# Kernel optimization log

Hardware: AMD Instinct MI355X
Metric: run time of the kernel (lower is better)

The kernel has to match this reference:

```python
import jax, jax.numpy as jnp
import numpy as np

DIM_IN = 1024
DIM_OUT = 1024
BATCH = 4
SEQ = 2048


def setup_inputs() -> dict:
    key = jax.random.key(0)
    kx, kq, kk, kv = jax.random.split(key, 4)
    scale = 1.0 / np.sqrt(DIM_IN)
    x = jax.random.normal(kx, (BATCH, SEQ, DIM_IN), dtype=jnp.float32)
    # Weights stored as [dim_in, dim_out] (transpose of torch Linear's [out, in]);
    # y = x @ W is equivalent math to torch's x @ W_t.T
    Wq = jax.random.normal(kq, (DIM_IN, DIM_OUT), dtype=jnp.float32) * scale
    Wk = jax.random.normal(kk, (DIM_IN, DIM_OUT), dtype=jnp.float32) * scale
    Wv = jax.random.normal(kv, (DIM_IN, DIM_OUT), dtype=jnp.float32) * scale
    return {"x": x, "Wq": Wq, "Wk": Wk, "Wv": Wv}


def reference(x, Wq, Wk, Wv):
    # x: [b, s, d_in]; single-head causal self-attention (dropout=0 -> identity)
    q = jnp.einsum("bsd,de->bse", x, Wq)
    k = jnp.einsum("bsd,de->bse", x, Wk)
    v = jnp.einsum("bsd,de->bse", x, Wv)
    dim_k = k.shape[-1]
    scores = jnp.einsum("bqe,bke->bqk", q, k) / jnp.sqrt(jnp.float32(dim_k))
    s = x.shape[1]
    causal = jnp.tril(jnp.ones((s, s), dtype=bool))  # True = keep
    scores = jnp.where(causal[None, :, :], scores, -jnp.inf)
    weights = jax.nn.softmax(scores, axis=-1)
    context = jnp.einsum("bqk,bke->bqe", weights, v)
    return context
```

## Files before the change

kernel.cpp:

```cpp
#include <hip/hip_runtime.h>
#include <cstdint>
#include <cstddef>
#include <type_traits>

typedef unsigned short u16;
typedef __bf16 bf16x8 __attribute__((ext_vector_type(8)));
typedef float f32x4 __attribute__((ext_vector_type(4)));

__device__ inline u16 f2b(float f) {
    uint32_t u = __builtin_bit_cast(uint32_t, f);
    u += 0x7FFFu + ((u >> 16) & 1u);
    return (u16)(u >> 16);
}

__device__ inline void gl2lds16(const u16* g, u16* l) {
    __builtin_amdgcn_global_load_lds(
        (const __attribute__((address_space(1))) void*)g,
        (__attribute__((address_space(3))) void*)l, 16, 0, 0);
}

template<int N> __device__ __forceinline__ void waitvm() {
    asm volatile("s_waitcnt vmcnt(%0)" :: "n"(N) : "memory");
}
__device__ __forceinline__ void bar() {
    asm volatile("" ::: "memory");
    __builtin_amdgcn_s_barrier();
    asm volatile("" ::: "memory");
}

__global__ void convert_x_kernel(const float* __restrict__ x, u16* __restrict__ xb) {
    size_t i = ((size_t)blockIdx.x * 256 + threadIdx.x) * 4;
    float4 v = *(const float4*)(x + i);
    uint2 pack;
    pack.x = (uint32_t)f2b(v.x) | ((uint32_t)f2b(v.y) << 16);
    pack.y = (uint32_t)f2b(v.z) | ((uint32_t)f2b(v.w) << 16);
    *(uint2*)(xb + i) = pack;
}

__global__ void transpose_w_kernel(const float* __restrict__ Wq,
                                   const float* __restrict__ Wk,
                                   const float* __restrict__ Wv,
                                   u16* __restrict__ QKWT, u16* __restrict__ WvT) {
    __shared__ u16 t[32][33];
    const int z = blockIdx.z;
    const float* W = (z == 0) ? Wq : ((z == 1) ? Wk : Wv);
    u16* dst = (z == 0) ? QKWT : ((z == 1) ? QKWT + 1024 * 1024 : WvT);
    const float scale = (z == 0) ? 0.03125f : 1.0f;
    const int bx = blockIdx.x * 32;
    const int by = blockIdx.y * 32;
    const int tx = threadIdx.x, ty = threadIdx.y;
    #pragma unroll
    for (int r = 0; r < 32; r += 8)
        t[ty + r][tx] = f2b(W[(size_t)(by + ty + r) * 1024 + bx + tx] * scale);
    __syncthreads();
    #pragma unroll
    for (int r = 0; r < 32; r += 8)
        dst[(size_t)(bx + ty + r) * 1024 + (by + tx)] = t[tx][ty + r];
}

template<int NB, int EPI>
__device__ __forceinline__ void gemm8p(
    char* __restrict__ sm,
    const u16* __restrict__ A, int lda,
    const u16* __restrict__ B, int ldb,
    char* __restrict__ Cb, int ldc,
    int m0, int n0, int Kloc, float* __restrict__ lrow)
{
    constexpr int BREG  = NB / 2;
    constexpr int BUFSZ = (2 + BREG) * 16384;
    constexpr int BOFF  = 2 * 16384;
    constexpr int WVM   = NB;

    const int tid  = threadIdx.x;
    const int lane = tid & 63, wave = tid >> 6;
    const int wm = wave >> 2, wn = wave & 3;
    const int fl = lane & 15, fh = lane >> 4;

    const int sx = ((fl & 4) << 3) ^ ((fl & 1) << 6);

    const int rr0 = tid >> 3;
    const int kc  = ((tid & 7) * 8) ^ ((rr0 & 4) << 2) ^ ((rr0 & 1) << 5);
    const u16* sA0a = A + (size_t)(m0 + rr0) * lda + kc;
    const u16* sA0b = A + (size_t)(m0 + rr0 + 64) * lda + kc;
    const u16* sA1a = sA0a + (size_t)128 * lda;
    const u16* sA1b = sA0b + (size_t)128 * lda;
    const u16* sB0a = B + (size_t)(n0 + rr0) * ldb + kc;
    const u16* sB0b = B + (size_t)(n0 + rr0 + 64) * ldb + kc;
    const u16* sB1a = sB0a + (size_t)128 * ldb;
    const u16* sB1b = sB0b + (size_t)128 * ldb;

    auto st = [&](const u16* s0, const u16* s1, int reg, int t) {
        u16* d = (u16*)(void*)(sm + (size_t)(t & 1) * BUFSZ + reg * 16384)
                 + wave * 512;
        gl2lds16(s0 + (size_t)t * 64, d);
        gl2lds16(s1 + (size_t)t * 64, d + 4096);
    };

    const f32x4 vzero = {0.f, 0.f, 0.f, 0.f};
    f32x4 acc[8][NB];
    #pragma unroll
    for (int i = 0; i < 8; ++i)
        #pragma unroll
        for (int j = 0; j < NB; ++j) acc[i][j] = vzero;

    const int NT = Kloc >> 6;
    const int NPAIR = NT >> 1;

    st(sB0a, sB0b, 2, 0);
    if constexpr (NB == 4) st(sB1a, sB1b, 3, 0);
    st(sA0a, sA0b, 0, 0);
    st(sA1a, sA1b, 1, 0);
    st(sB0a, sB0b, 2, 1);
    if constexpr (NB == 4) st(sB1a, sB1b, 3, 1);
    waitvm<WVM>();
    bar();

    bf16x8 bfrag[NB][2];
    for (int pr = 0; pr < NPAIR; ++pr) {
        const int t0 = pr * 2;
        const bool last = (pr == NPAIR - 1);

        auto phase = [&](auto phc) {
            constexpr int PH = decltype(phc)::value;
            constexpr int q = PH & 3;
            constexpr int b = PH >> 2;
            if constexpr (q == 0) {
                #pragma unroll
                for (int nt = 0; nt < NB; ++nt)
                    #pragma unroll
                    for (int kk = 0; kk < 2; ++kk)
                        bfrag[nt][kk] = *(const bf16x8*)(sm + b * BUFSZ + BOFF
                            + wn * (NB * 2048) + nt * 2048 + fl * 128
                            + ((fh * 16 + kk * 64) ^ sx));
            }
            bf16x8 af[2][2];
            #pragma unroll
            for (int i = 0; i < 2; ++i)
                #pragma unroll
                for (int kk = 0; kk < 2; ++kk)
                    af[i][kk] = *(const bf16x8*)(sm + b * BUFSZ + wm * 16384
                        + (q * 2 + i) * 2048 + fl * 128
                        + ((fh * 16 + kk * 64) ^ sx));
            if constexpr (PH == 0) { st(sA0a, sA0b, 0, t0 + 1);
                                     st(sA1a, sA1b, 1, t0 + 1); }
            if constexpr (PH == 1) { if (!last) st(sB0a, sB0b, 2, t0 + 2); }
            if constexpr (PH == 2 && NB == 4) { if (!last) st(sB1a, sB1b, 3, t0 + 2); }
            if constexpr (PH == 4) { if (!last) st(sA0a, sA0b, 0, t0 + 2); }
            if constexpr (PH == 5) { if (!last) st(sA1a, sA1b, 1, t0 + 2); }
            if constexpr (PH == 6) { if (!last) st(sB0a, sB0b, 2, t0 + 3); }
            if constexpr (PH == 7 && NB == 4) { if (!last) st(sB1a, sB1b, 3, t0 + 3); }
            if constexpr (PH == 3) { if (last) waitvm<0>(); else waitvm<WVM>(); }
            if constexpr (PH == 7) { if (!last) waitvm<WVM>(); }
            bar();
            __builtin_amdgcn_s_setprio(1);
            #pragma unroll
            for (int i = 0; i < 2; ++i)
                #pragma unroll
                for (int nt = 0; nt < NB; ++nt)
                    #pragma unroll
                    for (int kk = 0; kk < 2; ++kk)
                        acc[q * 2 + i][nt] = __builtin_amdgcn_mfma_f32_16x16x32_bf16(
                            af[i][kk], bfrag[nt][kk], acc[q * 2 + i][nt], 0, 0, 0);
            __builtin_amdgcn_s_setprio(0);
            bar();
        };
        phase(std::integral_constant<int, 0>{});
        phase(std::integral_constant<int, 1>{});
        phase(std::integral_constant<int, 2>{});
        phase(std::integral_constant<int, 3>{});
        phase(std::integral_constant<int, 4>{});
        phase(std::integral_constant<int, 5>{});
        phase(std::integral_constant<int, 6>{});
        phase(std::integral_constant<int, 7>{});
    }

    const int rbase = m0 + wm * 128 + fh * 4;
    const int cbase = n0 + wn * (NB * 16) + fl;
    if constexpr (EPI == 0) {
        u16* Cp = (u16*)Cb;
        #pragma unroll
        for (int mt = 0; mt < 8; ++mt)
            #pragma unroll
            for (int nt = 0; nt < NB; ++nt)
                #pragma unroll
                for (int r = 0; r < 4; ++r)
                    Cp[(size_t)(rbase + mt * 16 + r) * ldc + cbase + nt * 16] =
                        f2b(acc[mt][nt][r]);
    } else if constexpr (EPI == 2) {
        u16* Cp = (u16*)Cb;
        #pragma unroll
        for (int mt = 0; mt < 8; ++mt)
            #pragma unroll
            for (int r = 0; r < 4; ++r) {
                const int row = rbase + mt * 16 + r;
                float part = 0.f;
                #pragma unroll
                for (int nt = 0; nt < NB; ++nt) {
                    const int col = cbase + nt * 16;
                    float p = (col <= row) ? __expf(acc[mt][nt][r]) : 0.f;
                    part += p;
                    Cp[(size_t)row * ldc + col] = f2b(p);
                }
                #pragma unroll
                for (int off = 1; off < 16; off <<= 1)
                    part += __shfl_xor(part, off, 64);
                if (fl == 0) atomicAdd(lrow + row, part);
            }
    } else {
        float* Cp = (float*)Cb;
        #pragma unroll
        for (int mt = 0; mt < 8; ++mt)
            #pragma unroll
            for (int r = 0; r < 4; ++r) {
                const int row = rbase + mt * 16 + r;
                const float inv = 1.0f / lrow[row];
                #pragma unroll
                for (int nt = 0; nt < NB; ++nt)
                    Cp[(size_t)row * ldc + cbase + nt * 16] = acc[mt][nt][r] * inv;
            }
    }
}

__global__ __launch_bounds__(512, 2)
void proj_kernel(const u16* __restrict__ xb, const u16* __restrict__ QKWT,
                 const u16* __restrict__ WvT, u16* __restrict__ QK,
                 u16* __restrict__ Vt) {
    __shared__ __align__(16) char smem[131072];
    const int bid = ((int)blockIdx.x & 7) * 48 + ((int)blockIdx.x >> 3);
    const u16 *A, *B;
    char* C;
    int ldc, m0, n0;
    if (bid < 256) {
        const int it = bid >> 3, jt = bid & 7;
        A = xb;  B = QKWT;  C = (char*)QK;  ldc = 2048;
        m0 = it * 256;  n0 = jt * 256;
    } else {
        const int b = bid - 256;
        const int it = b >> 5, jt = b & 31;
        A = WvT;  B = xb;  C = (char*)Vt;  ldc = 8192;
        m0 = it * 256;  n0 = jt * 256;
    }
    gemm8p<4, 0>(smem, A, 1024, B, 1024, C, ldc, m0, n0, 1024, nullptr);
}

__global__ __launch_bounds__(512, 2)
void scores_kernel(const u16* __restrict__ QK, u16* __restrict__ P,
                   float* __restrict__ l) {
    __shared__ __align__(16) char smem[131072];
    const int t = blockIdx.x, z = blockIdx.y;
    int it = (int)((sqrtf(8.0f * t + 1.0f) - 1.0f) * 0.5f);
    while ((it + 1) * (it + 2) / 2 <= t) ++it;
    while (it * (it + 1) / 2 > t) --it;
    const int jt = t - it * (it + 1) / 2;
    const u16* Qz = QK + (size_t)z * 2048 * 2048;
    const u16* Kz = Qz + 1024;
    u16* Pz = P + (size_t)z * 2048 * 2048;
    gemm8p<4, 2>(smem, Qz, 2048, Kz, 2048, (char*)Pz, 2048,
                 it * 256, jt * 256, 1024, l + (size_t)z * 2048);
}

__global__ __launch_bounds__(512, 2)
void out_kernel(const u16* __restrict__ P, const u16* __restrict__ Vt,
                float* __restrict__ out, float* __restrict__ l) {
    __shared__ __align__(16) char smem[98304];
    const int jt = blockIdx.x;
    const int it = 7 - (int)blockIdx.y;
    const int z = blockIdx.z;
    gemm8p<2, 3>(smem, P + (size_t)z * 2048 * 2048, 2048,
                 Vt + (size_t)z * 2048, 8192,
                 (char*)(out + (size_t)z * 2048 * 1024), 1024,
                 it * 256, jt * 128, (it + 1) * 256, l + (size_t)z * 2048);
}

extern "C" void kernel_launch(void* const* d_in, const int* in_sizes, int n_in,
                              void* d_out, int out_size, void* d_ws, size_t ws_size,
                              hipStream_t stream) {
    (void)in_sizes; (void)n_in; (void)out_size; (void)ws_size;
    const float* x  = (const float*)d_in[0];
    const float* Wq = (const float*)d_in[1];
    const float* Wk = (const float*)d_in[2];
    const float* Wv = (const float*)d_in[3];
    float* out = (float*)d_out;

    const size_t MB = 1u << 20;
    char* ws = (char*)d_ws;
    u16* xb   = (u16*)(ws);
    u16* QKWT = (u16*)(ws + 16 * MB);
    u16* WvT  = (u16*)(ws + 20 * MB);
    u16* QK   = (u16*)(ws + 22 * MB);
    u16* Vt   = (u16*)(ws + 54 * MB);
    u16* P    = (u16*)(ws + 70 * MB);
    float* l  = (float*)(ws + 102 * MB);

    hipMemsetAsync(l, 0, 8192 * sizeof(float), stream);
    convert_x_kernel<<<8192, 256, 0, stream>>>(x, xb);
    transpose_w_kernel<<<dim3(32, 32, 3), dim3(32, 8), 0, stream>>>(Wq, Wk, Wv, QKWT, WvT);

    proj_kernel<<<384, 512, 0, stream>>>(xb, QKWT, WvT, QK, Vt);
    scores_kernel<<<dim3(36, 4), 512, 0, stream>>>(QK, P, l);
    out_kernel<<<dim3(8, 8, 4), 512, 0, stream>>>(P, Vt, out, l);
}
```

Before: 238.2 us.

## Split-K for long causal rows in PV GEMM, retile V projection, restructure phase barriers

The output GEMM now splits the K dimension in two for the four longest row tiles and accumulates them with atomic float adds into a zeroed output. This is meant to balance the causal triangle's uneven work across CUs. The V projection uses 256x128 tiles with 512 blocks and a new block swizzle for more parallelism. The pipeline phase now waits on LDS reads before a single barrier, then issues the next stores and the MFMAs without a trailing barrier. In exchange it adds an output memset, atomic traffic and nondeterministic summation order.

```diff
diff --git a/kernel.cpp b/kernel.cpp
--- a/kernel.cpp
+++ b/kernel.cpp
@@ -21,6 +21,9 @@
 
 template<int N> __device__ __forceinline__ void waitvm() {
     asm volatile("s_waitcnt vmcnt(%0)" :: "n"(N) : "memory");
+}
+__device__ __forceinline__ void waitlgkm0() {
+    asm volatile("s_waitcnt lgkmcnt(0)" ::: "memory");
 }
 __device__ __forceinline__ void bar() {
     asm volatile("" ::: "memory");
@@ -141,6 +144,10 @@
                     af[i][kk] = *(const bf16x8*)(sm + b * BUFSZ + wm * 16384
                         + (q * 2 + i) * 2048 + fl * 128
                         + ((fh * 16 + kk * 64) ^ sx));
+            if constexpr (PH == 3) { if (last) waitvm<0>(); else waitvm<WVM>(); }
+            if constexpr (PH == 7) { if (!last) waitvm<WVM>(); }
+            waitlgkm0();
+            bar();
             if constexpr (PH == 0) { st(sA0a, sA0b, 0, t0 + 1);
                                      st(sA1a, sA1b, 1, t0 + 1); }
             if constexpr (PH == 1) { if (!last) st(sB0a, sB0b, 2, t0 + 2); }
@@ -149,9 +156,6 @@
             if constexpr (PH == 5) { if (!last) st(sA1a, sA1b, 1, t0 + 2); }
             if constexpr (PH == 6) { if (!last) st(sB0a, sB0b, 2, t0 + 3); }
             if constexpr (PH == 7 && NB == 4) { if (!last) st(sB1a, sB1b, 3, t0 + 3); }
-            if constexpr (PH == 3) { if (last) waitvm<0>(); else waitvm<WVM>(); }
-            if constexpr (PH == 7) { if (!last) waitvm<WVM>(); }
-            bar();
             __builtin_amdgcn_s_setprio(1);
             #pragma unroll
             for (int i = 0; i < 2; ++i)
@@ -162,7 +166,6 @@
                         acc[q * 2 + i][nt] = __builtin_amdgcn_mfma_f32_16x16x32_bf16(
                             af[i][kk], bfrag[nt][kk], acc[q * 2 + i][nt], 0, 0, 0);
             __builtin_amdgcn_s_setprio(0);
-            bar();
         };
         phase(std::integral_constant<int, 0>{});
         phase(std::integral_constant<int, 1>{});
@@ -206,7 +209,7 @@
                     part += __shfl_xor(part, off, 64);
                 if (fl == 0) atomicAdd(lrow + row, part);
             }
-    } else {
+    } else if constexpr (EPI == 3) {
         float* Cp = (float*)Cb;
         #pragma unroll
         for (int mt = 0; mt < 8; ++mt)
@@ -217,6 +220,19 @@
                 #pragma unroll
                 for (int nt = 0; nt < NB; ++nt)
                     Cp[(size_t)row * ldc + cbase + nt * 16] = acc[mt][nt][r] * inv;
+            }
+    } else {
+        float* Cp = (float*)Cb;
+        #pragma unroll
+        for (int mt = 0; mt < 8; ++mt)
+            #pragma unroll
+            for (int r = 0; r < 4; ++r) {
+                const int row = rbase + mt * 16 + r;
+                const float inv = 1.0f / lrow[row];
+                #pragma unroll
+                for (int nt = 0; nt < NB; ++nt)
+                    atomicAdd(&Cp[(size_t)row * ldc + cbase + nt * 16],
+                              acc[mt][nt][r] * inv);
             }
     }
 }
@@ -226,21 +242,19 @@
                  const u16* __restrict__ WvT, u16* __restrict__ QK,
                  u16* __restrict__ Vt) {
     __shared__ __align__(16) char smem[131072];
-    const int bid = ((int)blockIdx.x & 7) * 48 + ((int)blockIdx.x >> 3);
-    const u16 *A, *B;
-    char* C;
-    int ldc, m0, n0;
-    if (bid < 256) {
+    const int x = (int)blockIdx.x;
+    if (x < 256) {
+        const int bid = (x & 7) * 32 + (x >> 3);
         const int it = bid >> 3, jt = bid & 7;
-        A = xb;  B = QKWT;  C = (char*)QK;  ldc = 2048;
-        m0 = it * 256;  n0 = jt * 256;
+        gemm8p<4, 0>(smem, xb, 1024, QKWT, 1024, (char*)QK, 2048,
+                     it * 256, jt * 256, 1024, nullptr);
     } else {
-        const int b = bid - 256;
-        const int it = b >> 5, jt = b & 31;
-        A = WvT;  B = xb;  C = (char*)Vt;  ldc = 8192;
-        m0 = it * 256;  n0 = jt * 256;
+        const int y = x - 256;
+        const int bid = (y & 7) * 32 + (y >> 3);
+        const int it = bid >> 6, jt = bid & 63;
+        gemm8p<2, 0>(smem, WvT, 1024, xb, 1024, (char*)Vt, 8192,
+                     it * 256, jt * 128, 1024, nullptr);
     }
-    gemm8p<4, 0>(smem, A, 1024, B, 1024, C, ldc, m0, n0, 1024, nullptr);
 }
 
 __global__ __launch_bounds__(512, 2)
@@ -263,13 +277,25 @@
 void out_kernel(const u16* __restrict__ P, const u16* __restrict__ Vt,
                 float* __restrict__ out, float* __restrict__ l) {
     __shared__ __align__(16) char smem[98304];
-    const int jt = blockIdx.x;
-    const int it = 7 - (int)blockIdx.y;
-    const int z = blockIdx.z;
-    gemm8p<2, 3>(smem, P + (size_t)z * 2048 * 2048, 2048,
-                 Vt + (size_t)z * 2048, 8192,
-                 (char*)(out + (size_t)z * 2048 * 1024), 1024,
-                 it * 256, jt * 128, (it + 1) * 256, l + (size_t)z * 2048);
+    const int o = (int)blockIdx.x;
+    int it, half, split, r;
+    if (o < 256) { const int pc = o >> 5; r = o & 31; it = 7 - (pc >> 1);
+                   half = pc & 1; split = 1; }
+    else         { const int pc = (o - 256) >> 5; r = o & 31; it = 3 - pc;
+                   half = 0; split = 0; }
+    const int jt = r & 7, z = r >> 3;
+    const int Kloc = split ? (it + 1) * 128 : (it + 1) * 256;
+    const int k0 = half * Kloc;
+    const u16* Pz = P + (size_t)z * 2048 * 2048 + k0;
+    const u16* Vz = Vt + (size_t)z * 2048 + k0;
+    char* C = (char*)(out + (size_t)z * 2048 * 1024);
+    float* lz = l + (size_t)z * 2048;
+    if (split)
+        gemm8p<2, 4>(smem, Pz, 2048, Vz, 8192, C, 1024,
+                     it * 256, jt * 128, Kloc, lz);
+    else
+        gemm8p<2, 3>(smem, Pz, 2048, Vz, 8192, C, 1024,
+                     it * 256, jt * 128, Kloc, lz);
 }
 
 extern "C" void kernel_launch(void* const* d_in, const int* in_sizes, int n_in,
@@ -293,10 +319,11 @@
     float* l  = (float*)(ws + 102 * MB);
 
     hipMemsetAsync(l, 0, 8192 * sizeof(float), stream);
+    hipMemsetAsync(out, 0, (size_t)4 * 2048 * 1024 * sizeof(float), stream);
     convert_x_kernel<<<8192, 256, 0, stream>>>(x, xb);
     transpose_w_kernel<<<dim3(32, 32, 3), dim3(32, 8), 0, stream>>>(Wq, Wk, Wv, QKWT, WvT);
 
-    proj_kernel<<<384, 512, 0, stream>>>(xb, QKWT, WvT, QK, Vt);
+    proj_kernel<<<512, 512, 0, stream>>>(xb, QKWT, WvT, QK, Vt);
     scores_kernel<<<dim3(36, 4), 512, 0, stream>>>(QK, P, l);
-    out_kernel<<<dim3(8, 8, 4), 512, 0, stream>>>(P, Vt, out, l);
-}
+    out_kernel<<<384, 512, 0, stream>>>(P, Vt, out, l);
+}
```

New measurement: 254.5 us. +6.9%, slower.
